# Optimization experiments

Measured on AMD Instinct MI355X. Metric: run time of the kernel, lower is better.

## Reference

```python
import jax, jax.numpy as jnp
import numpy as np

B, L, HID, NH, HD = 1, 2304, 3072, 24, 128
IMG = 2048
MLP = 4 * HID  # 12288
EPS = 1e-6


def _layernorm(x):
    mu = jnp.mean(x, axis=-1, keepdims=True)
    var = jnp.mean(jnp.square(x - mu), axis=-1, keepdims=True)
    return (x - mu) * jax.lax.rsqrt(var + EPS)


def _rmsnorm(x, w):
    ms = jnp.mean(jnp.square(x), axis=-1, keepdims=True)
    return x * jax.lax.rsqrt(ms + EPS) * w


def _rope_interleaved(x, cos, sin):
    # x: [B, S, H, D]; cos/sin: [1, S, 1, D] with pairwise-equal values (mode=1, GPT-J)
    x1 = x[..., 0::2]
    x2 = x[..., 1::2]
    c = cos[..., 0::2]
    s = sin[..., 0::2]
    even = x1 * c - x2 * s
    odd = x1 * s + x2 * c
    return jnp.stack([even, odd], axis=-1).reshape(x.shape)


def setup_inputs() -> dict:
    key = jax.random.key(0)
    ks = jax.random.split(key, 10)
    scale_in = 1.0 / np.sqrt(HID)
    x = jax.random.normal(ks[0], (B, L, HID), jnp.float32)
    vec = jax.random.normal(ks[1], (B, HID), jnp.float32)
    # RoPE tables (interleaved layout: value repeated per pair)
    pos = jnp.arange(IMG, dtype=jnp.float32)
    inv_freq = 1.0 / (10000.0 ** (jnp.arange(HD // 2, dtype=jnp.float32) / (HD // 2)))
    ang = pos[:, None] * inv_freq[None, :]               # [IMG, HD/2]
    freqs_cos = jnp.repeat(jnp.cos(ang), 2, axis=-1).reshape(1, IMG, 1, HD)
    freqs_sin = jnp.repeat(jnp.sin(ang), 2, axis=-1).reshape(1, IMG, 1, HD)
    mod_w = jax.random.normal(ks[2], (HID, 3 * HID), jnp.float32) * scale_in
    mod_b = jnp.zeros((3 * HID,), jnp.float32)
    w1 = jax.random.normal(ks[3], (HID, 3 * HID + MLP), jnp.float32) * scale_in
    b1 = jnp.zeros((3 * HID + MLP,), jnp.float32)
    q_norm_w = jnp.ones((HD,), jnp.float32)
    k_norm_w = jnp.ones((HD,), jnp.float32)
    w2 = jax.random.normal(ks[4], (HID + MLP, HID), jnp.float32) * (1.0 / np.sqrt(HID + MLP))
    b2 = jnp.zeros((HID,), jnp.float32)
    return {
        'x': x, 'vec': vec, 'img_len': IMG,
        'freqs_cos': freqs_cos, 'freqs_sin': freqs_sin,
        'mod_w': mod_w, 'mod_b': mod_b, 'w1': w1, 'b1': b1,
        'q_norm_w': q_norm_w, 'k_norm_w': k_norm_w, 'w2': w2, 'b2': b2,
    }


def reference(x, vec, img_len, freqs_cos, freqs_sin, mod_w, mod_b, w1, b1,
              q_norm_w, k_norm_w, w2, b2):
    # modulation: SiLU(vec) -> Linear -> shift/scale/gate  [B, HID] each
    mod = jax.nn.silu(vec) @ mod_w + mod_b
    shift, scale, gate = jnp.split(mod, 3, axis=-1)
    x_mod = _layernorm(x) * (1.0 + scale[:, None, :]) + shift[:, None, :]

    # fused QKV + MLP projection
    proj = x_mod @ w1 + b1                                  # [B, L, 3*HID + MLP]
    qkv, mlp = proj[..., :3 * HID], proj[..., 3 * HID:]
    q, k, v = [t[:, :, 0] for t in [None]] if False else None, None, None
    qkv = qkv.reshape(B, L, 3, NH, HD)
    q, k, v = qkv[:, :, 0], qkv[:, :, 1], qkv[:, :, 2]      # [B, L, NH, HD]

    q = _rmsnorm(q, q_norm_w)
    k = _rmsnorm(k, k_norm_w)

    # RoPE only on image tokens
    q = jnp.concatenate([_rope_interleaved(q[:, :img_len], freqs_cos, freqs_sin), q[:, img_len:]], axis=1)
    k = jnp.concatenate([_rope_interleaved(k[:, :img_len], freqs_cos, freqs_sin), k[:, img_len:]], axis=1)

    # full (img+txt) bidirectional attention
    attn_scale = 1.0 / np.sqrt(HD)
    scores = jnp.einsum('blhd,bmhd->bhlm', q, k) * attn_scale
    probs = jax.nn.softmax(scores, axis=-1)
    attn = jnp.einsum('bhlm,bmhd->blhd', probs, v).reshape(B, L, NH * HD)

    # output fusion: [attn | gelu_tanh(mlp)] @ w2
    out = jnp.concatenate([attn, jax.nn.gelu(mlp, approximate=True)], axis=-1) @ w2 + b2
    return x + out * gate[:, None, :]
```

## Files before the change

### kernel.cpp

```cpp
#include <hip/hip_runtime.h>

#define L_SEQ 2304
#define HID_D 3072
#define NH_D 24
#define HD_D 128
#define N1_D 21504
#define QKVN 9216
#define K2_D 15360
#define EPS_V 1e-6f
#define ATTN_SC 0.08838834764831843f

typedef __bf16 bf16x8 __attribute__((ext_vector_type(8)));
typedef float f32x4 __attribute__((ext_vector_type(4)));
typedef unsigned int u32x4 __attribute__((ext_vector_type(4)));
typedef unsigned short u16x8 __attribute__((ext_vector_type(8)));
typedef unsigned short u16x4 __attribute__((ext_vector_type(4)));

__device__ __forceinline__ unsigned short f2bf(float f) {
  unsigned int u = __builtin_bit_cast(unsigned int, f);
  u += 0x7fffu + ((u >> 16) & 1u);
  return (unsigned short)(u >> 16);
}

__device__ __forceinline__ float gelu_f(float x) {
  float u = 0.7978845608028654f * (x + 0.044715f * x * x * x);
  float e = __expf(2.f * u);
  float th = 1.f - 2.f / (e + 1.f);
  return 0.5f * x * (1.f + th);
}

__device__ __forceinline__ void gload16(const void* g, void* l) {
  __builtin_amdgcn_global_load_lds(
      (const __attribute__((address_space(1))) unsigned int*)g,
      (__attribute__((address_space(3))) unsigned int*)l, 16, 0, 0);
}

__global__ __launch_bounds__(256) void mod_partial_kernel(
    const float* __restrict__ vec, const float* __restrict__ mod_w,
    float* __restrict__ partial) {
  __shared__ float s[384];
  const int t = threadIdx.x;
  const int kb = blockIdx.y;
  const int k0 = kb * 384;
  for (int p = t; p < 384; p += 256) {
    float v = vec[k0 + p];
    s[p] = v / (1.f + __expf(-v));
  }
  __syncthreads();
  const int n = blockIdx.x * 256 + t;
  float acc = 0.f;
  const float* wp = mod_w + (size_t)k0 * QKVN + n;
#pragma unroll 4
  for (int j = 0; j < 384; ++j) acc += s[j] * wp[(size_t)j * QKVN];
  partial[kb * QKVN + n] = acc;
}

__global__ __launch_bounds__(256) void mod_reduce_kernel(
    const float* __restrict__ partial, const float* __restrict__ mod_b,
    float* __restrict__ mod) {
  const int n = blockIdx.x * 256 + threadIdx.x;
  float acc = mod_b[n];
#pragma unroll
  for (int i = 0; i < 8; ++i) acc += partial[i * QKVN + n];
  mod[n] = acc;
}

__global__ __launch_bounds__(256) void ln_mod_kernel(
    const float* __restrict__ x, const float* __restrict__ mod,
    unsigned short* __restrict__ xmod) {
  const int row = blockIdx.x;
  const int t = threadIdx.x;
  const float* xr = x + (size_t)row * HID_D;
  float4 v[3];
  float sum = 0.f, sq = 0.f;
#pragma unroll
  for (int p = 0; p < 3; ++p) {
    v[p] = *(const float4*)&xr[p * 1024 + t * 4];
    sum += v[p].x + v[p].y + v[p].z + v[p].w;
    sq += v[p].x * v[p].x + v[p].y * v[p].y + v[p].z * v[p].z + v[p].w * v[p].w;
  }
#pragma unroll
  for (int o = 1; o < 64; o <<= 1) {
    sum += __shfl_xor(sum, o);
    sq += __shfl_xor(sq, o);
  }
  __shared__ float rs[8];
  const int w = t >> 6;
  if ((t & 63) == 0) { rs[w] = sum; rs[4 + w] = sq; }
  __syncthreads();
  sum = rs[0] + rs[1] + rs[2] + rs[3];
  sq = rs[4] + rs[5] + rs[6] + rs[7];
  const float mu = sum * (1.f / HID_D);
  const float var = sq * (1.f / HID_D) - mu * mu;
  const float rstd = rsqrtf(var + EPS_V);
#pragma unroll
  for (int p = 0; p < 3; ++p) {
    const int c = p * 1024 + t * 4;
    float4 sc = *(const float4*)&mod[3072 + c];
    float4 sh = *(const float4*)&mod[c];
    u16x4 o4;
    o4[0] = f2bf((v[p].x - mu) * rstd * (1.f + sc.x) + sh.x);
    o4[1] = f2bf((v[p].y - mu) * rstd * (1.f + sc.y) + sh.y);
    o4[2] = f2bf((v[p].z - mu) * rstd * (1.f + sc.z) + sh.z);
    o4[3] = f2bf((v[p].w - mu) * rstd * (1.f + sc.w) + sh.w);
    *(u16x4*)&xmod[(size_t)row * HID_D + c] = o4;
  }
}

__global__ __launch_bounds__(256) void convert_transpose_kernel(
    const float* __restrict__ src, unsigned short* __restrict__ dst,
    const int K, const int N) {
  __shared__ unsigned short lt[64][72];
  const int t = threadIdx.x;
  const int n0 = blockIdx.x * 64;
  const int k0 = blockIdx.y * 64;
  const int kr = t >> 4;
  const int n4 = (t & 15) * 4;
#pragma unroll
  for (int p = 0; p < 4; ++p) {
    const int k = kr + p * 16;
    float4 v = *(const float4*)&src[(size_t)(k0 + k) * N + n0 + n4];
    lt[n4 + 0][k] = f2bf(v.x);
    lt[n4 + 1][k] = f2bf(v.y);
    lt[n4 + 2][k] = f2bf(v.z);
    lt[n4 + 3][k] = f2bf(v.w);
  }
  __syncthreads();
  const int nr = t >> 2;
  const int kc = (t & 3) * 16;
  u16x8 a = *(const u16x8*)&lt[nr][kc];
  u16x8 b = *(const u16x8*)&lt[nr][kc + 8];
  unsigned short* dp = &dst[(size_t)(n0 + nr) * K + k0 + kc];
  *(u16x8*)dp = a;
  *(u16x8*)(dp + 8) = b;
}

__device__ __forceinline__ void gemm_pipe(
    const unsigned short* __restrict__ A, const int lda,
    const unsigned short* __restrict__ B, const int ldb,
    const int m0, const int n0, const int nk,
    unsigned short* lds_a, unsigned short* lds_b, f32x4 acc[4][4]) {
  const int t = threadIdx.x;
  const int lane = t & 63;
  const int w = t >> 6;
  const int g = lane >> 4;
  const int c = lane & 15;
  const int wr = (w >> 1) * 64;
  const int wc = (w & 1) * 64;

  const int srow = w * 8 + (lane >> 3);
  const int scol = ((lane & 7) ^ (lane >> 3)) * 8;
  const unsigned short* gA = A + (size_t)(m0 + srow) * lda + scol;
  const unsigned short* gB = B + (size_t)(n0 + srow) * ldb + scol;
  unsigned short* lA = lds_a + w * 512;
  unsigned short* lB = lds_b + w * 512;

  auto stage = [&](int buf, int kt) {
    const size_t ko = (size_t)kt * 64;
#pragma unroll
    for (int i = 0; i < 4; ++i) {
      gload16(gA + (size_t)i * 32 * lda + ko, lA + buf * 8192 + i * 2048);
      gload16(gB + (size_t)i * 32 * ldb + ko, lB + buf * 8192 + i * 2048);
    }
  };

  auto compute = [&](int buf) {
    const char* bA = (const char*)(lds_a + buf * 8192);
    const char* bB = (const char*)(lds_b + buf * 8192);
#pragma unroll
    for (int kk = 0; kk < 2; ++kk) {
      bf16x8 af[4], bfr[4];
#pragma unroll
      for (int mf = 0; mf < 4; ++mf) {
        const int m = wr + mf * 16 + c;
        af[mf] = *(const bf16x8*)(bA + ((m * 128 + kk * 64 + g * 16) ^ ((c & 7) << 4)));
      }
#pragma unroll
      for (int nf = 0; nf < 4; ++nf) {
        const int n = wc + nf * 16 + c;
        bfr[nf] = *(const bf16x8*)(bB + ((n * 128 + kk * 64 + g * 16) ^ ((c & 7) << 4)));
      }
      __builtin_amdgcn_s_setprio(1);
#pragma unroll
      for (int mf = 0; mf < 4; ++mf)
#pragma unroll
        for (int nf = 0; nf < 4; ++nf)
          acc[mf][nf] = __builtin_amdgcn_mfma_f32_16x16x32_bf16(af[mf], bfr[nf],
                                                                acc[mf][nf], 0, 0, 0);
      __builtin_amdgcn_s_setprio(0);
    }
  };

  stage(0, 0);
  stage(1, 1);
  asm volatile("s_waitcnt vmcnt(8)" ::: "memory");
  __builtin_amdgcn_s_barrier();
  asm volatile("" ::: "memory");

  for (int kt = 0; kt < nk; ++kt) {
    const int cur = kt & 1;
    compute(cur);
    asm volatile("s_waitcnt lgkmcnt(0)" ::: "memory");
    __builtin_amdgcn_s_barrier();
    asm volatile("" ::: "memory");
    if (kt + 2 < nk) {
      stage(cur, kt + 2);
      asm volatile("s_waitcnt vmcnt(8)" ::: "memory");
    } else {
      asm volatile("s_waitcnt vmcnt(0)" ::: "memory");
    }
    __builtin_amdgcn_s_barrier();
    asm volatile("" ::: "memory");
  }
}

__global__ __launch_bounds__(256) void gemm1_kernel(
    const unsigned short* __restrict__ xmod, const unsigned short* __restrict__ w1t,
    const float* __restrict__ b1, float* __restrict__ qkv,
    unsigned short* __restrict__ hbuf) {
  __shared__ unsigned short lds_a[2 * 128 * 64];
  __shared__ unsigned short lds_b[2 * 128 * 64];
  f32x4 acc[4][4];
  const f32x4 zero = {0.f, 0.f, 0.f, 0.f};
#pragma unroll
  for (int i = 0; i < 4; ++i)
#pragma unroll
    for (int j = 0; j < 4; ++j) acc[i][j] = zero;
  int bid = blockIdx.x;
  bid = (bid & 7) * (18 * 168 / 8) + (bid >> 3);
  const int m0 = (bid % 18) * 128;
  const int n0 = (bid / 18) * 128;
  gemm_pipe(xmod, HID_D, w1t, HID_D, m0, n0, HID_D / 64, lds_a, lds_b, acc);
  const int lane = threadIdx.x & 63;
  const int g = lane >> 4, c = lane & 15;
  const int w = threadIdx.x >> 6;
  const int wr = (w >> 1) * 64, wc = (w & 1) * 64;
  const bool is_mlp = (n0 >= QKVN);
#pragma unroll
  for (int mf = 0; mf < 4; ++mf)
#pragma unroll
    for (int nf = 0; nf < 4; ++nf)
#pragma unroll
      for (int j = 0; j < 4; ++j) {
        const int row = m0 + wr + mf * 16 + g * 4 + j;
        const int col = n0 + wc + nf * 16 + c;
        const float v = acc[mf][nf][j] + b1[col];
        if (!is_mlp) {
          qkv[(size_t)row * QKVN + col] = v;
        } else {
          hbuf[(size_t)row * K2_D + HID_D + (col - QKVN)] = f2bf(gelu_f(v));
        }
      }
}

__global__ __launch_bounds__(256) void gemm2_kernel(
    const unsigned short* __restrict__ hbuf, const unsigned short* __restrict__ w2t,
    const float* __restrict__ b2, const float* __restrict__ x,
    const float* __restrict__ mod, float* __restrict__ out) {
  __shared__ unsigned short lds_a[2 * 128 * 64];
  __shared__ unsigned short lds_b[2 * 128 * 64];
  f32x4 acc[4][4];
  const f32x4 zero = {0.f, 0.f, 0.f, 0.f};
#pragma unroll
  for (int i = 0; i < 4; ++i)
#pragma unroll
    for (int j = 0; j < 4; ++j) acc[i][j] = zero;
  int bid = blockIdx.x;
  bid = (bid & 7) * (18 * 24 / 8) + (bid >> 3);
  const int m0 = (bid % 18) * 128;
  const int n0 = (bid / 18) * 128;
  gemm_pipe(hbuf, K2_D, w2t, K2_D, m0, n0, K2_D / 64, lds_a, lds_b, acc);
  const int lane = threadIdx.x & 63;
  const int g = lane >> 4, c = lane & 15;
  const int w = threadIdx.x >> 6;
  const int wr = (w >> 1) * 64, wc = (w & 1) * 64;
#pragma unroll
  for (int mf = 0; mf < 4; ++mf)
#pragma unroll
    for (int nf = 0; nf < 4; ++nf)
#pragma unroll
      for (int j = 0; j < 4; ++j) {
        const int row = m0 + wr + mf * 16 + g * 4 + j;
        const int col = n0 + wc + nf * 16 + c;
        const float v = acc[mf][nf][j] + b2[col];
        out[(size_t)row * HID_D + col] =
            x[(size_t)row * HID_D + col] + v * mod[6144 + col];
      }
}

__global__ __launch_bounds__(256) void qk_norm_rope_kernel(
    const float* __restrict__ qkv, const float* __restrict__ qw,
    const float* __restrict__ kw, const float* __restrict__ fc,
    const float* __restrict__ fs, const int* __restrict__ img_len_p,
    unsigned short* __restrict__ qr, unsigned short* __restrict__ kr) {
  const int l = blockIdx.x;
  const int t = threadIdx.x;
  const int wv = t >> 6;
  const int lane = t & 63;
  const int img = *img_len_p;
  const bool do_rope = (l < img);
  float cc = 1.f, ss = 0.f;
  if (do_rope) {
    cc = fc[l * HD_D + 2 * lane];
    ss = fs[l * HD_D + 2 * lane];
  }
  const float qw0 = qw[2 * lane], qw1 = qw[2 * lane + 1];
  const float kw0 = kw[2 * lane], kw1 = kw[2 * lane + 1];
#pragma unroll
  for (int hh = 0; hh < 6; ++hh) {
    const int h = hh * 4 + wv;
    {
      float2 q2 = *(const float2*)&qkv[(size_t)l * QKVN + h * HD_D + 2 * lane];
      float sq = q2.x * q2.x + q2.y * q2.y;
#pragma unroll
      for (int o = 1; o < 64; o <<= 1) sq += __shfl_xor(sq, o);
      const float r = rsqrtf(sq * (1.f / HD_D) + EPS_V);
      float a = q2.x * r * qw0, b = q2.y * r * qw1;
      float e = a, od = b;
      if (do_rope) { e = a * cc - b * ss; od = a * ss + b * cc; }
      e *= ATTN_SC; od *= ATTN_SC;
      unsigned int pk = (unsigned)f2bf(e) | ((unsigned)f2bf(od) << 16);
      *(unsigned int*)&qr[((size_t)h * L_SEQ + l) * HD_D + 2 * lane] = pk;
    }
    {
      float2 k2 = *(const float2*)&qkv[(size_t)l * QKVN + HID_D + h * HD_D + 2 * lane];
      float sq = k2.x * k2.x + k2.y * k2.y;
#pragma unroll
      for (int o = 1; o < 64; o <<= 1) sq += __shfl_xor(sq, o);
      const float r = rsqrtf(sq * (1.f / HD_D) + EPS_V);
      float a = k2.x * r * kw0, b = k2.y * r * kw1;
      float e = a, od = b;
      if (do_rope) { e = a * cc - b * ss; od = a * ss + b * cc; }
      unsigned int pk = (unsigned)f2bf(e) | ((unsigned)f2bf(od) << 16);
      *(unsigned int*)&kr[((size_t)h * L_SEQ + l) * HD_D + 2 * lane] = pk;
    }
  }
}

__global__ __launch_bounds__(256) void v_transpose_kernel(
    const float* __restrict__ qkv, unsigned short* __restrict__ vT) {
  __shared__ unsigned short lv[128 * 64];
  const int h = blockIdx.y;
  const int l0 = blockIdx.x * 64;
  const int t = threadIdx.x;
#pragma unroll
  for (int p = 0; p < 8; ++p) {
    const int idx = p * 256 + t;
    const int l = idx >> 5;
    const int d4 = (idx & 31) * 4;
    float4 v = *(const float4*)&qkv[(size_t)(l0 + l) * QKVN + 2 * HID_D + h * HD_D + d4];
    const unsigned sw = (unsigned)(((d4 >> 2) & 7) << 4);
    *(unsigned short*)((char*)lv + (((d4 + 0) * 128 + 2 * l) ^ sw)) = f2bf(v.x);
    *(unsigned short*)((char*)lv + (((d4 + 1) * 128 + 2 * l) ^ sw)) = f2bf(v.y);
    *(unsigned short*)((char*)lv + (((d4 + 2) * 128 + 2 * l) ^ sw)) = f2bf(v.z);
    *(unsigned short*)((char*)lv + (((d4 + 3) * 128 + 2 * l) ^ sw)) = f2bf(v.w);
  }
  __syncthreads();
  const int d = t >> 1;
  const int half = t & 1;
  const unsigned swr = (unsigned)(((d >> 2) & 7) << 4);
#pragma unroll
  for (int j2 = 0; j2 < 4; ++j2) {
    u32x4 v = *(const u32x4*)((const char*)lv + ((d * 128 + half * 64 + j2 * 16) ^ swr));
    *(u32x4*)&vT[(size_t)(h * HD_D + d) * L_SEQ + l0 + half * 32 + j2 * 8] = v;
  }
}

__global__ __launch_bounds__(256) void attn_kernel(
    const unsigned short* __restrict__ qr, const unsigned short* __restrict__ kr,
    const unsigned short* __restrict__ vT, unsigned short* __restrict__ hbuf) {
  __shared__ unsigned short lds_k[64 * 128];
  __shared__ unsigned short lds_v[128 * 64];
  __shared__ unsigned short lds_p[4 * 16 * 64];
  const int hidx = blockIdx.y;
  const int l0 = blockIdx.x * 64;
  const int t = threadIdx.x;
  const int lane = t & 63;
  const int w = t >> 6;
  const int g = lane >> 4;
  const int c = lane & 15;

  bf16x8 qa[4];
  {
    const unsigned short* qrow = qr + ((size_t)hidx * L_SEQ + l0 + w * 16 + c) * HD_D;
#pragma unroll
    for (int ks = 0; ks < 4; ++ks)
      qa[ks] = *(const bf16x8*)&qrow[ks * 32 + g * 8];
  }
  f32x4 acc[8];
  const f32x4 zero = {0.f, 0.f, 0.f, 0.f};
#pragma unroll
  for (int i = 0; i < 8; ++i) acc[i] = zero;
  float m_r[4] = {-1e30f, -1e30f, -1e30f, -1e30f};
  float l_r[4] = {0.f, 0.f, 0.f, 0.f};

  for (int kv0 = 0; kv0 < L_SEQ; kv0 += 64) {
    __syncthreads();
#pragma unroll
    for (int p = 0; p < 4; ++p) {
      const int idx = p * 256 + t;
      const int r = idx >> 4, ch = idx & 15;
      u32x4 v = *(const u32x4*)&kr[((size_t)hidx * L_SEQ + kv0 + r) * HD_D + ch * 8];
      *(u32x4*)((char*)lds_k + ((r * 256 + ch * 16) ^ ((r & 7) << 4))) = v;
    }
#pragma unroll
    for (int p = 0; p < 4; ++p) {
      const int idx = p * 256 + t;
      const int d_ = idx >> 3, ch = idx & 7;
      u32x4 v = *(const u32x4*)&vT[(size_t)(hidx * HD_D + d_) * L_SEQ + kv0 + ch * 8];
      *(u32x4*)((char*)lds_v + ((d_ * 128 + ch * 16) ^ ((d_ & 7) << 4))) = v;
    }
    __syncthreads();
    f32x4 s[4];
#pragma unroll
    for (int cf = 0; cf < 4; ++cf) s[cf] = zero;
#pragma unroll
    for (int ks = 0; ks < 4; ++ks) {
      const int kb = (ks * 32 + g * 8) * 2;
#pragma unroll
      for (int cf = 0; cf < 4; ++cf) {
        const int kvr = cf * 16 + c;
        bf16x8 kf = *(const bf16x8*)((const char*)lds_k + ((kvr * 256 + kb) ^ ((kvr & 7) << 4)));
        s[cf] = __builtin_amdgcn_mfma_f32_16x16x32_bf16(qa[ks], kf, s[cf], 0, 0, 0);
      }
    }
    float pv[4][4];
    float alpha[4];
#pragma unroll
    for (int r = 0; r < 4; ++r) {
      float mx = fmaxf(fmaxf(s[0][r], s[1][r]), fmaxf(s[2][r], s[3][r]));
      mx = fmaxf(mx, __shfl_xor(mx, 1));
      mx = fmaxf(mx, __shfl_xor(mx, 2));
      mx = fmaxf(mx, __shfl_xor(mx, 4));
      mx = fmaxf(mx, __shfl_xor(mx, 8));
      const float mnew = fmaxf(m_r[r], mx);
      alpha[r] = __expf(m_r[r] - mnew);
      float rsum = 0.f;
#pragma unroll
      for (int cf = 0; cf < 4; ++cf) {
        const float p_ = __expf(s[cf][r] - mnew);
        pv[cf][r] = p_;
        rsum += p_;
      }
      rsum += __shfl_xor(rsum, 1);
      rsum += __shfl_xor(rsum, 2);
      rsum += __shfl_xor(rsum, 4);
      rsum += __shfl_xor(rsum, 8);
      l_r[r] = l_r[r] * alpha[r] + rsum;
      m_r[r] = mnew;
    }
#pragma unroll
    for (int of = 0; of < 8; ++of)
#pragma unroll
      for (int r = 0; r < 4; ++r) acc[of][r] *= alpha[r];
#pragma unroll
    for (int cf = 0; cf < 4; ++cf)
#pragma unroll
      for (int r = 0; r < 4; ++r) {
        const int row = g * 4 + r;
        const int col = cf * 16 + c;
        *(unsigned short*)((char*)lds_p +
                           ((w * 2048 + row * 128 + col * 2) ^ ((row & 7) << 4))) =
            f2bf(pv[cf][r]);
      }
    asm volatile("s_waitcnt lgkmcnt(0)" ::: "memory");
    __builtin_amdgcn_sched_barrier(0);
#pragma unroll
    for (int ks = 0; ks < 2; ++ks) {
      bf16x8 pa = *(const bf16x8*)((const char*)lds_p +
                                   ((w * 2048 + c * 128 + (ks * 32 + g * 8) * 2) ^
                                    ((c & 7) << 4)));
#pragma unroll
      for (int of = 0; of < 8; ++of) {
        const int dcol = of * 16 + c;
        bf16x8 vb = *(const bf16x8*)((const char*)lds_v +
                                     ((dcol * 128 + (ks * 32 + g * 8) * 2) ^
                                      ((dcol & 7) << 4)));
        acc[of] = __builtin_amdgcn_mfma_f32_16x16x32_bf16(pa, vb, acc[of], 0, 0, 0);
      }
    }
  }
#pragma unroll
  for (int of = 0; of < 8; ++of)
#pragma unroll
    for (int r = 0; r < 4; ++r) {
      const int row = l0 + w * 16 + g * 4 + r;
      const int col = hidx * HD_D + of * 16 + c;
      hbuf[(size_t)row * K2_D + col] = f2bf(acc[of][r] / l_r[r]);
    }
}

extern "C" void kernel_launch(void* const* d_in, const int* in_sizes, int n_in,
                              void* d_out, int out_size, void* d_ws, size_t ws_size,
                              hipStream_t stream) {
  (void)in_sizes; (void)n_in; (void)out_size; (void)ws_size;
  const float* x = (const float*)d_in[0];
  const float* vec = (const float*)d_in[1];
  const int* img_len = (const int*)d_in[2];
  const float* fc = (const float*)d_in[3];
  const float* fs = (const float*)d_in[4];
  const float* mod_w = (const float*)d_in[5];
  const float* mod_b = (const float*)d_in[6];
  const float* w1 = (const float*)d_in[7];
  const float* b1 = (const float*)d_in[8];
  const float* qw = (const float*)d_in[9];
  const float* kw = (const float*)d_in[10];
  const float* w2 = (const float*)d_in[11];
  const float* b2 = (const float*)d_in[12];
  float* out = (float*)d_out;

  char* wsb = (char*)d_ws;
  float* mod = (float*)(wsb + 0);
  float* partial = (float*)(wsb + 36864);
  unsigned short* xmod = (unsigned short*)(wsb + 331776);
  float* qkv = (float*)(wsb + 14487552);
  unsigned short* hbuf = (unsigned short*)(wsb + 99422208);
  unsigned short* qr = (unsigned short*)(wsb + 170201088);
  unsigned short* kr = (unsigned short*)(wsb + 184356864);
  unsigned short* vT = (unsigned short*)(wsb + 198512640);
  unsigned short* wt = (unsigned short*)(wsb + 212668416);

  mod_partial_kernel<<<dim3(36, 8), 256, 0, stream>>>(vec, mod_w, partial);
  mod_reduce_kernel<<<36, 256, 0, stream>>>(partial, mod_b, mod);
  ln_mod_kernel<<<2304, 256, 0, stream>>>(x, mod, xmod);
  convert_transpose_kernel<<<dim3(N1_D / 64, HID_D / 64), 256, 0, stream>>>(
      w1, wt, HID_D, N1_D);
  gemm1_kernel<<<18 * 168, 256, 0, stream>>>(xmod, wt, b1, qkv, hbuf);
  convert_transpose_kernel<<<dim3(HID_D / 64, K2_D / 64), 256, 0, stream>>>(
      w2, wt, K2_D, HID_D);
  qk_norm_rope_kernel<<<2304, 256, 0, stream>>>(qkv, qw, kw, fc, fs, img_len, qr, kr);
  v_transpose_kernel<<<dim3(36, 24), 256, 0, stream>>>(qkv, vT);
  attn_kernel<<<dim3(36, 24), 256, 0, stream>>>(qr, kr, vT, hbuf);
  gemm2_kernel<<<18 * 24, 256, 0, stream>>>(hbuf, wt, b2, x, mod, out);
}
```

Before: 1.148 ms.

## Widen GEMM tiles to 128x256 with 8 waves and triple-buffered LDS pipeline

Both projection GEMMs move from 128x128 tiles with 4 waves to 128x256 tiles with 8 waves per block, so each A tile is reused across twice as many output columns. The K-loop becomes a three-buffer LDS ring, and the next-next stage is issued between the two k-halves of each iteration rather than after a full compute plus extra barrier. This aims to cut global and LDS traffic per FLOP and hide load latency better. The larger LDS footprint (about 144KB) likely limits residency to one block per CU, and gemm2 drops to 216 blocks, fewer than the CU count, so some CUs sit idle.

```diff
diff --git a/kernel.cpp b/kernel.cpp
--- a/kernel.cpp
+++ b/kernel.cpp
@@ -135,50 +135,62 @@
   *(u16x8*)(dp + 8) = b;
 }
 
-__device__ __forceinline__ void gemm_pipe(
+__device__ __forceinline__ void gemm_core2(
     const unsigned short* __restrict__ A, const int lda,
     const unsigned short* __restrict__ B, const int ldb,
-    const int m0, const int n0, const int nk,
-    unsigned short* lds_a, unsigned short* lds_b, f32x4 acc[4][4]) {
+    const int m0, const int n0, const int nt,
+    unsigned short* ldsA, unsigned short* ldsB, f32x4 acc[4][4]) {
   const int t = threadIdx.x;
   const int lane = t & 63;
   const int w = t >> 6;
   const int g = lane >> 4;
   const int c = lane & 15;
-  const int wr = (w >> 1) * 64;
-  const int wc = (w & 1) * 64;
-
-  const int srow = w * 8 + (lane >> 3);
-  const int scol = ((lane & 7) ^ (lane >> 3)) * 8;
-  const unsigned short* gA = A + (size_t)(m0 + srow) * lda + scol;
-  const unsigned short* gB = B + (size_t)(n0 + srow) * ldb + scol;
-  unsigned short* lA = lds_a + w * 512;
-  unsigned short* lB = lds_b + w * 512;
+  const int wm = (w >> 2) * 64;
+  const int wn = (w & 3) * 64;
+
+  const int sr = lane >> 3;
+  const int scol = ((lane & 7) ^ sr) * 8;
+
+  const unsigned short* ga[2];
+  const unsigned short* gb[4];
+#pragma unroll
+  for (int j = 0; j < 2; ++j)
+    ga[j] = A + (size_t)(m0 + (j * 8 + w) * 8 + sr) * lda + scol;
+#pragma unroll
+  for (int j = 0; j < 4; ++j)
+    gb[j] = B + (size_t)(n0 + (j * 8 + w) * 8 + sr) * ldb + scol;
 
   auto stage = [&](int buf, int kt) {
     const size_t ko = (size_t)kt * 64;
 #pragma unroll
-    for (int i = 0; i < 4; ++i) {
-      gload16(gA + (size_t)i * 32 * lda + ko, lA + buf * 8192 + i * 2048);
-      gload16(gB + (size_t)i * 32 * ldb + ko, lB + buf * 8192 + i * 2048);
-    }
+    for (int j = 0; j < 2; ++j)
+      gload16(ga[j] + ko, ldsA + buf * 8192 + (j * 8 + w) * 512);
+#pragma unroll
+    for (int j = 0; j < 4; ++j)
+      gload16(gb[j] + ko, ldsB + buf * 16384 + (j * 8 + w) * 512);
   };
 
-  auto compute = [&](int buf) {
-    const char* bA = (const char*)(lds_a + buf * 8192);
-    const char* bB = (const char*)(lds_b + buf * 8192);
-#pragma unroll
-    for (int kk = 0; kk < 2; ++kk) {
+  stage(0, 0);
+  stage(1, 1);
+  asm volatile("s_waitcnt vmcnt(6)" ::: "memory");
+  __builtin_amdgcn_s_barrier();
+  asm volatile("" ::: "memory");
+
+  int bt = 0, bs = 2;
+  for (int kt = 0; kt < nt; ++kt) {
+    const char* bA = (const char*)(ldsA + bt * 8192);
+    const char* bB = (const char*)(ldsB + bt * 16384);
+    {
       bf16x8 af[4], bfr[4];
 #pragma unroll
       for (int mf = 0; mf < 4; ++mf) {
-        const int m = wr + mf * 16 + c;
-        af[mf] = *(const bf16x8*)(bA + ((m * 128 + kk * 64 + g * 16) ^ ((c & 7) << 4)));
+        const int m = wm + mf * 16 + c;
+        af[mf] = *(const bf16x8*)(bA + ((m * 128 + g * 16) ^ ((m & 7) << 4)));
       }
 #pragma unroll
       for (int nf = 0; nf < 4; ++nf) {
-        const int n = wc + nf * 16 + c;
-        bfr[nf] = *(const bf16x8*)(bB + ((n * 128 + kk * 64 + g * 16) ^ ((c & 7) << 4)));
+        const int n = wn + nf * 16 + c;
+        bfr[nf] = *(const bf16x8*)(bB + ((n * 128 + g * 16) ^ ((n & 7) << 4)));
       }
       __builtin_amdgcn_s_setprio(1);
 #pragma unroll
@@ -189,37 +201,48 @@
                                                                 acc[mf][nf], 0, 0, 0);
       __builtin_amdgcn_s_setprio(0);
     }
-  };
-
-  stage(0, 0);
-  stage(1, 1);
-  asm volatile("s_waitcnt vmcnt(8)" ::: "memory");
-  __builtin_amdgcn_s_barrier();
-  asm volatile("" ::: "memory");
-
-  for (int kt = 0; kt < nk; ++kt) {
-    const int cur = kt & 1;
-    compute(cur);
-    asm volatile("s_waitcnt lgkmcnt(0)" ::: "memory");
     __builtin_amdgcn_s_barrier();
     asm volatile("" ::: "memory");
-    if (kt + 2 < nk) {
-      stage(cur, kt + 2);
-      asm volatile("s_waitcnt vmcnt(8)" ::: "memory");
-    } else {
+    if (kt + 2 < nt) stage(bs, kt + 2);
+    {
+      bf16x8 af[4], bfr[4];
+#pragma unroll
+      for (int mf = 0; mf < 4; ++mf) {
+        const int m = wm + mf * 16 + c;
+        af[mf] = *(const bf16x8*)(bA + ((m * 128 + 64 + g * 16) ^ ((m & 7) << 4)));
+      }
+#pragma unroll
+      for (int nf = 0; nf < 4; ++nf) {
+        const int n = wn + nf * 16 + c;
+        bfr[nf] = *(const bf16x8*)(bB + ((n * 128 + 64 + g * 16) ^ ((n & 7) << 4)));
+      }
+      __builtin_amdgcn_s_setprio(1);
+#pragma unroll
+      for (int mf = 0; mf < 4; ++mf)
+#pragma unroll
+        for (int nf = 0; nf < 4; ++nf)
+          acc[mf][nf] = __builtin_amdgcn_mfma_f32_16x16x32_bf16(af[mf], bfr[nf],
+                                                                acc[mf][nf], 0, 0, 0);
+      __builtin_amdgcn_s_setprio(0);
+    }
+    if (kt + 2 < nt) {
+      asm volatile("s_waitcnt vmcnt(6)" ::: "memory");
+    } else if (kt + 1 < nt) {
       asm volatile("s_waitcnt vmcnt(0)" ::: "memory");
     }
     __builtin_amdgcn_s_barrier();
     asm volatile("" ::: "memory");
-  }
-}
-
-__global__ __launch_bounds__(256) void gemm1_kernel(
+    bt = (bt == 2) ? 0 : bt + 1;
+    bs = (bs == 2) ? 0 : bs + 1;
+  }
+}
+
+__global__ __launch_bounds__(512, 2) void gemm1_kernel(
     const unsigned short* __restrict__ xmod, const unsigned short* __restrict__ w1t,
     const float* __restrict__ b1, float* __restrict__ qkv,
     unsigned short* __restrict__ hbuf) {
-  __shared__ unsigned short lds_a[2 * 128 * 64];
-  __shared__ unsigned short lds_b[2 * 128 * 64];
+  __shared__ unsigned short ldsA[3 * 8192];
+  __shared__ unsigned short ldsB[3 * 16384];
   f32x4 acc[4][4];
   const f32x4 zero = {0.f, 0.f, 0.f, 0.f};
 #pragma unroll
@@ -227,14 +250,14 @@
 #pragma unroll
     for (int j = 0; j < 4; ++j) acc[i][j] = zero;
   int bid = blockIdx.x;
-  bid = (bid & 7) * (18 * 168 / 8) + (bid >> 3);
+  bid = (bid & 7) * (1512 / 8) + (bid >> 3);
   const int m0 = (bid % 18) * 128;
-  const int n0 = (bid / 18) * 128;
-  gemm_pipe(xmod, HID_D, w1t, HID_D, m0, n0, HID_D / 64, lds_a, lds_b, acc);
+  const int n0 = (bid / 18) * 256;
+  gemm_core2(xmod, HID_D, w1t, HID_D, m0, n0, HID_D / 64, ldsA, ldsB, acc);
   const int lane = threadIdx.x & 63;
   const int g = lane >> 4, c = lane & 15;
   const int w = threadIdx.x >> 6;
-  const int wr = (w >> 1) * 64, wc = (w & 1) * 64;
+  const int wm = (w >> 2) * 64, wn = (w & 3) * 64;
   const bool is_mlp = (n0 >= QKVN);
 #pragma unroll
   for (int mf = 0; mf < 4; ++mf)
@@ -242,8 +265,8 @@
     for (int nf = 0; nf < 4; ++nf)
 #pragma unroll
       for (int j = 0; j < 4; ++j) {
-        const int row = m0 + wr + mf * 16 + g * 4 + j;
-        const int col = n0 + wc + nf * 16 + c;
+        const int row = m0 + wm + mf * 16 + g * 4 + j;
+        const int col = n0 + wn + nf * 16 + c;
         const float v = acc[mf][nf][j] + b1[col];
         if (!is_mlp) {
           qkv[(size_t)row * QKVN + col] = v;
@@ -253,12 +276,12 @@
       }
 }
 
-__global__ __launch_bounds__(256) void gemm2_kernel(
+__global__ __launch_bounds__(512, 2) void gemm2_kernel(
     const unsigned short* __restrict__ hbuf, const unsigned short* __restrict__ w2t,
     const float* __restrict__ b2, const float* __restrict__ x,
     const float* __restrict__ mod, float* __restrict__ out) {
-  __shared__ unsigned short lds_a[2 * 128 * 64];
-  __shared__ unsigned short lds_b[2 * 128 * 64];
+  __shared__ unsigned short ldsA[3 * 8192];
+  __shared__ unsigned short ldsB[3 * 16384];
   f32x4 acc[4][4];
   const f32x4 zero = {0.f, 0.f, 0.f, 0.f};
 #pragma unroll
@@ -266,22 +289,22 @@
 #pragma unroll
     for (int j = 0; j < 4; ++j) acc[i][j] = zero;
   int bid = blockIdx.x;
-  bid = (bid & 7) * (18 * 24 / 8) + (bid >> 3);
+  bid = (bid & 7) * (216 / 8) + (bid >> 3);
   const int m0 = (bid % 18) * 128;
-  const int n0 = (bid / 18) * 128;
-  gemm_pipe(hbuf, K2_D, w2t, K2_D, m0, n0, K2_D / 64, lds_a, lds_b, acc);
+  const int n0 = (bid / 18) * 256;
+  gemm_core2(hbuf, K2_D, w2t, K2_D, m0, n0, K2_D / 64, ldsA, ldsB, acc);
   const int lane = threadIdx.x & 63;
   const int g = lane >> 4, c = lane & 15;
   const int w = threadIdx.x >> 6;
-  const int wr = (w >> 1) * 64, wc = (w & 1) * 64;
+  const int wm = (w >> 2) * 64, wn = (w & 3) * 64;
 #pragma unroll
   for (int mf = 0; mf < 4; ++mf)
 #pragma unroll
     for (int nf = 0; nf < 4; ++nf)
 #pragma unroll
       for (int j = 0; j < 4; ++j) {
-        const int row = m0 + wr + mf * 16 + g * 4 + j;
-        const int col = n0 + wc + nf * 16 + c;
+        const int row = m0 + wm + mf * 16 + g * 4 + j;
+        const int col = n0 + wn + nf * 16 + c;
         const float v = acc[mf][nf][j] + b2[col];
         out[(size_t)row * HID_D + col] =
             x[(size_t)row * HID_D + col] + v * mod[6144 + col];
@@ -525,11 +548,11 @@
   ln_mod_kernel<<<2304, 256, 0, stream>>>(x, mod, xmod);
   convert_transpose_kernel<<<dim3(N1_D / 64, HID_D / 64), 256, 0, stream>>>(
       w1, wt, HID_D, N1_D);
-  gemm1_kernel<<<18 * 168, 256, 0, stream>>>(xmod, wt, b1, qkv, hbuf);
+  gemm1_kernel<<<18 * 84, 512, 0, stream>>>(xmod, wt, b1, qkv, hbuf);
   convert_transpose_kernel<<<dim3(HID_D / 64, K2_D / 64), 256, 0, stream>>>(
       w2, wt, K2_D, HID_D);
   qk_norm_rope_kernel<<<2304, 256, 0, stream>>>(qkv, qw, kw, fc, fs, img_len, qr, kr);
   v_transpose_kernel<<<dim3(36, 24), 256, 0, stream>>>(qkv, vT);
   attn_kernel<<<dim3(36, 24), 256, 0, stream>>>(qr, kr, vT, hbuf);
-  gemm2_kernel<<<18 * 24, 256, 0, stream>>>(hbuf, wt, b2, x, mod, out);
-}
+  gemm2_kernel<<<18 * 12, 512, 0, stream>>>(hbuf, wt, b2, x, mod, out);
+}
```

Result: slower. 1.398 ms (+21.8%).
